# Optimization experiments

Measured on AMD Instinct MI355X. Metric: run time of the kernel, lower is better.

Reference implementation:

```python
import jax, jax.numpy as jnp
import numpy as np

DIM = 1024
HEADS = 16
HIDDEN = 4096
EPS = 1e-5


def layernorm(x, w, b):
    mu = jnp.mean(x, axis=-1, keepdims=True)
    var = jnp.var(x, axis=-1, keepdims=True)
    return (x - mu) * jax.lax.rsqrt(var + EPS) * w + b


def setup_inputs() -> dict:
    key = jax.random.key(0)
    ks = jax.random.split(key, 12)
    s = lambda fan_in: 1.0 / np.sqrt(fan_in)
    return {
        "x": jax.random.normal(ks[0], (8, 1024, DIM), dtype=jnp.float32),
        "norm1_w": jnp.ones((DIM,), jnp.float32),
        "norm1_b": jnp.zeros((DIM,), jnp.float32),
        "qkv_w": jax.random.uniform(ks[1], (3 * DIM, DIM), jnp.float32, -s(DIM), s(DIM)),
        "proj_w": jax.random.uniform(ks[2], (DIM, DIM), jnp.float32, -s(DIM), s(DIM)),
        "proj_b": jax.random.uniform(ks[3], (DIM,), jnp.float32, -s(DIM), s(DIM)),
        "norm2_w": jnp.ones((DIM,), jnp.float32),
        "norm2_b": jnp.zeros((DIM,), jnp.float32),
        "fc1_w": jax.random.uniform(ks[4], (HIDDEN, DIM), jnp.float32, -s(DIM), s(DIM)),
        "fc1_b": jax.random.uniform(ks[5], (HIDDEN,), jnp.float32, -s(DIM), s(DIM)),
        "fc2_w": jax.random.uniform(ks[6], (DIM, HIDDEN), jnp.float32, -s(HIDDEN), s(HIDDEN)),
        "fc2_b": jax.random.uniform(ks[7], (DIM,), jnp.float32, -s(HIDDEN), s(HIDDEN)),
    }


def reference(x, norm1_w, norm1_b, qkv_w, proj_w, proj_b,
              norm2_w, norm2_b, fc1_w, fc1_b, fc2_w, fc2_b):
    B, N, C = x.shape
    hd = C // HEADS
    scale = hd ** -0.5

    # ---- attention branch ----
    xn = layernorm(x, norm1_w, norm1_b)
    qkv_tmp = jnp.einsum('bnc,oc->bno', xn, qkv_w)          # [B,N,3C]
    qkv = qkv_tmp.reshape(B, N, 3, HEADS, hd).transpose(2, 0, 3, 1, 4)
    q, k, v = qkv[0], qkv[1], qkv[2]                         # [B,H,N,hd]
    qkv_out = qkv_tmp.reshape(B, N, 3, C).transpose(2, 0, 1, 3)
    attn = jnp.einsum('bhnd,bhmd->bhnm', q, k) * scale       # [B,H,N,N]
    attn = jax.nn.softmax(attn, axis=-1)
    ao = jnp.einsum('bhnm,bhmd->bhnd', attn, v)              # [B,H,N,hd]
    ao = ao.transpose(0, 2, 1, 3).reshape(B, N, C)
    attn_out = jnp.einsum('bnc,oc->bno', ao, proj_w) + proj_b
    x = x + attn_out

    # ---- mlp branch ----
    xn2 = layernorm(x, norm2_w, norm2_b)
    h = jnp.einsum('bnc,hc->bnh', xn2, fc1_w) + fc1_b
    h = jax.nn.gelu(h, approximate=False)
    hidden_out = jnp.einsum('bnh,ch->bnc', h, fc2_w) + fc2_b
    x = x + hidden_out
    return (x, (qkv_out[0], qkv_out[1], qkv_out[2]), hidden_out)
```

## Files before the change

### kernel.cpp

```cpp
#include <hip/hip_runtime.h>
#include <hip/hip_bf16.h>

typedef __attribute__((ext_vector_type(8))) __bf16 bf16x8;
typedef __attribute__((ext_vector_type(4))) float f32x4;
typedef unsigned short u16;
typedef unsigned int u32;

#define TOK 8192
#define C_DIM 1024
#define OUT_SEC 8388608

__device__ __forceinline__ u16 f2bf(float f) {
  return __builtin_bit_cast(u16, __float2bfloat16(f));
}

__device__ __forceinline__ void gl_lds16(const void* g, void* l) {
  __builtin_amdgcn_global_load_lds(
      (__attribute__((address_space(1))) void*)const_cast<void*>(g),
      (__attribute__((address_space(3))) void*)l, 16, 0, 0);
}

__device__ __forceinline__ float gelu_f(float x) {
  float y = 0.7978845608f * (x + 0.044715f * x * x * x);
  y = fminf(fmaxf(y, -15.f), 15.f);
  float e = __expf(2.0f * y);
  float th = (e - 1.0f) / (e + 1.0f);
  return 0.5f * x * (1.0f + th);
}

__global__ __launch_bounds__(256) void cvt_kernel(const float* __restrict__ in,
                                                  u16* __restrict__ out, int n4) {
  int i = blockIdx.x * blockDim.x + threadIdx.x;
  if (i >= n4) return;
  float4 v = reinterpret_cast<const float4*>(in)[i];
  alignas(8) u16 pk[4];
  pk[0] = f2bf(v.x); pk[1] = f2bf(v.y); pk[2] = f2bf(v.z); pk[3] = f2bf(v.w);
  reinterpret_cast<uint2*>(out)[i] = *reinterpret_cast<uint2*>(pk);
}

__global__ __launch_bounds__(256) void ln_kernel(const float* __restrict__ x,
                                                 const float* __restrict__ w,
                                                 const float* __restrict__ b,
                                                 u16* __restrict__ out) {
  const int row = blockIdx.x;
  const int t = threadIdx.x;
  const float* xr = x + (size_t)row * C_DIM;
  float4 v = reinterpret_cast<const float4*>(xr)[t];
  float s = v.x + v.y + v.z + v.w;
  float ss = v.x * v.x + v.y * v.y + v.z * v.z + v.w * v.w;
#pragma unroll
  for (int off = 1; off < 64; off <<= 1) {
    s += __shfl_xor(s, off, 64);
    ss += __shfl_xor(ss, off, 64);
  }
  __shared__ float red[8];
  const int wv = t >> 6;
  if ((t & 63) == 0) { red[wv] = s; red[4 + wv] = ss; }
  __syncthreads();
  s = red[0] + red[1] + red[2] + red[3];
  ss = red[4] + red[5] + red[6] + red[7];
  const float mu = s * (1.0f / C_DIM);
  const float var = ss * (1.0f / C_DIM) - mu * mu;
  const float rstd = rsqrtf(var + 1e-5f);
  float4 w4 = reinterpret_cast<const float4*>(w)[t];
  float4 b4 = reinterpret_cast<const float4*>(b)[t];
  alignas(8) u16 pk[4];
  pk[0] = f2bf((v.x - mu) * rstd * w4.x + b4.x);
  pk[1] = f2bf((v.y - mu) * rstd * w4.y + b4.y);
  pk[2] = f2bf((v.z - mu) * rstd * w4.z + b4.z);
  pk[3] = f2bf((v.w - mu) * rstd * w4.w + b4.w);
  reinterpret_cast<uint2*>(out + (size_t)row * C_DIM)[t] = *reinterpret_cast<uint2*>(pk);
}

__global__ __launch_bounds__(256) void vtrans_kernel(const float* __restrict__ vsrc,
                                                     u16* __restrict__ vt) {
  const int bh = blockIdx.x, nt = blockIdx.y;
  const int b = bh >> 4, h = bh & 15;
  const int t = threadIdx.x;
  __shared__ u16 T[64][65];
#pragma unroll
  for (int p = 0; p < 4; ++p) {
    const int idx = p * 256 + t;
    const int n = idx >> 4, d4 = (idx & 15) * 4;
    float4 x4 = *reinterpret_cast<const float4*>(
        vsrc + (size_t)(b * 1024 + nt * 64 + n) * 1024 + h * 64 + d4);
    T[d4 + 0][n] = f2bf(x4.x);
    T[d4 + 1][n] = f2bf(x4.y);
    T[d4 + 2][n] = f2bf(x4.z);
    T[d4 + 3][n] = f2bf(x4.w);
  }
  __syncthreads();
  const int d = t >> 2, ns = (t & 3) * 16;
  u16* dst = vt + (size_t)bh * 65536 + (size_t)d * 1024 + nt * 64 + ns;
  alignas(16) u16 tmp[16];
#pragma unroll
  for (int i = 0; i < 16; ++i) tmp[i] = T[d][ns + i];
  reinterpret_cast<uint4*>(dst)[0] = reinterpret_cast<uint4*>(tmp)[0];
  reinterpret_cast<uint4*>(dst)[1] = reinterpret_cast<uint4*>(tmp)[1];
}

#define MFMA_T(AF, BF, BASE)                                                \
  _Pragma("unroll") for (int nf = 0; nf < 4; ++nf) {                        \
    _Pragma("unroll") for (int mf = 0; mf < 4; ++mf)                        \
        acc[(BASE) + mf][nf] = __builtin_amdgcn_mfma_f32_16x16x32_bf16(     \
            AF[mf], BF[nf], acc[(BASE) + mf][nf], 0, 0, 0);                 \
  }

enum { EPI8_QKV = 0, EPI8_FC1 = 1 };

template <int EPI>
__global__ __launch_bounds__(512, 2) void gemm8(
    const u16* __restrict__ A, const u16* __restrict__ Bw,
    const float* __restrict__ bias,
    float* __restrict__ out, u16* __restrict__ h1, u16* __restrict__ h2,
    int K) {
  extern __shared__ char smem[];
  const int t = threadIdx.x, lane = t & 63, wid = t >> 6;
  const int wm = wid >> 2, wn = wid & 3;

  const int nwg = gridDim.x;
  int lin = blockIdx.x;
  lin = (lin & 7) * (nwg >> 3) + (lin >> 3);
  const int brow0 = (lin & 31) * 256;
  const int bcol0 = (lin >> 5) * 256;

  const int NT = K >> 6;

  f32x4 zero = {0.f, 0.f, 0.f, 0.f};
  f32x4 acc[8][4];
#pragma unroll
  for (int m = 0; m < 8; ++m)
#pragma unroll
    for (int n = 0; n < 4; ++n) acc[m][n] = zero;

  const int src_slot = ((t & 3) ^ ((t >> 3) & 3)) * 8;
  const int srow = t >> 2;
  auto stage = [&](int buf, int mat, int ks, int ktile) {
    const u16* G = mat ? Bw : A;
    const int gr0 = mat ? bcol0 : brow0;
    const int k0 = ktile * 64 + ks * 32 + src_slot;
    char* dst = smem + ((buf << 16) | (mat << 15) | (ks << 14));
#pragma unroll
    for (int i = 0; i < 2; ++i)
      gl_lds16(G + (size_t)(gr0 + i * 128 + srow) * K + k0, dst + i * 8192 + t * 16);
  };

  const int swz16 = (((lane >> 4) ^ ((lane >> 1) & 3)) << 4);
  const int l15 = lane & 15;

  stage(0, 0, 0, 0);
  stage(0, 1, 0, 0);
  stage(0, 0, 1, 0);
  stage(0, 1, 1, 0);
  asm volatile("s_waitcnt vmcnt(4)" ::: "memory");
  __builtin_amdgcn_s_barrier();

  for (int tt = 0; tt < NT; ++tt) {
    char* As_ = smem + ((tt & 1) << 16);
    char* Bs_ = As_ + 32768;
    const int nbuf = (tt & 1) ^ 1;
    const bool pf = (tt + 1 < NT);
    bf16x8 af[4], af2[4], bfr[4];

    auto LDA = [&](bf16x8* dst8, int MH, int KK) {
#pragma unroll
      for (int mf = 0; mf < 4; ++mf)
        dst8[mf] = *reinterpret_cast<const bf16x8*>(
            As_ + KK * 16384 + (wm * 128 + MH * 64 + mf * 16 + l15) * 64 + swz16);
    };
    auto LDB = [&](int KK) {
#pragma unroll
      for (int nf = 0; nf < 4; ++nf)
        bfr[nf] = *reinterpret_cast<const bf16x8*>(
            Bs_ + KK * 16384 + (wn * 64 + nf * 16 + l15) * 64 + swz16);
    };

    LDB(0);
    LDA(af, 0, 0);
    __builtin_amdgcn_sched_barrier(0);
    LDA(af2, 1, 0);
    __builtin_amdgcn_sched_barrier(0);
    if (pf) { stage(nbuf, 0, 0, tt + 1); stage(nbuf, 1, 0, tt + 1); }
    asm volatile("s_waitcnt lgkmcnt(4)" ::: "memory");
    __builtin_amdgcn_sched_barrier(0);
    __builtin_amdgcn_s_setprio(1);
    MFMA_T(af, bfr, 0)
    asm volatile("s_waitcnt lgkmcnt(0)" ::: "memory");
    __builtin_amdgcn_sched_barrier(0);
    MFMA_T(af2, bfr, 4)
    __builtin_amdgcn_s_setprio(0);
    if (pf) {
      asm volatile("s_waitcnt vmcnt(4)" ::: "memory");
    } else {
      asm volatile("s_waitcnt vmcnt(0)" ::: "memory");
    }
    __builtin_amdgcn_s_barrier();

    LDB(1);
    LDA(af, 1, 1);
    __builtin_amdgcn_sched_barrier(0);
    LDA(af2, 0, 1);
    __builtin_amdgcn_sched_barrier(0);
    if (pf) { stage(nbuf, 0, 1, tt + 1); stage(nbuf, 1, 1, tt + 1); }
    asm volatile("s_waitcnt lgkmcnt(4)" ::: "memory");
    __builtin_amdgcn_sched_barrier(0);
    __builtin_amdgcn_s_setprio(1);
    MFMA_T(af, bfr, 4)
    asm volatile("s_waitcnt lgkmcnt(0)" ::: "memory");
    __builtin_amdgcn_sched_barrier(0);
    MFMA_T(af2, bfr, 0)
    __builtin_amdgcn_s_setprio(0);
    if (pf)
      asm volatile("s_waitcnt vmcnt(4)" ::: "memory");
    __builtin_amdgcn_s_barrier();
  }

  const int rb = brow0 + wm * 128;
  const int cb = bcol0 + wn * 64;
#pragma unroll
  for (int m = 0; m < 8; ++m) {
#pragma unroll
    for (int n = 0; n < 4; ++n) {
      const int c = cb + n * 16 + l15;
#pragma unroll
      for (int j = 0; j < 4; ++j) {
        const int r = rb + m * 16 + (lane >> 4) * 4 + j;
        float v = acc[m][n][j];
        if constexpr (EPI == EPI8_QKV) {
          const int sec = c >> 10, cc = c & 1023;
          out[(size_t)sec * OUT_SEC + (size_t)r * 1024 + cc] = v;
          const size_t boff =
              (((size_t)(r >> 10) * 16 + (cc >> 6)) * 1024 + (r & 1023)) * 64 + (cc & 63);
          if (sec == 0) h1[boff] = f2bf(v * 0.18033688f);
          else if (sec == 1) h2[boff] = f2bf(v);
        } else {
          v += bias[c];
          h1[(size_t)r * 4096 + c] = f2bf(gelu_f(v));
        }
      }
    }
  }
}

enum { EPIN_PROJ = 0, EPIN_FC2 = 1 };

template <int EPI>
__global__ __launch_bounds__(512, 1) void gemm8n(
    const u16* __restrict__ A, const u16* __restrict__ Bw,
    const float* __restrict__ bias, const float* resid,
    float* out, float* out2_f, int K) {
  extern __shared__ char smem[];
  const int t = threadIdx.x, lane = t & 63, wid = t >> 6;
  const int wm = wid >> 2, wn = wid & 3;

  const int nwg = gridDim.x;
  int lin = blockIdx.x;
  lin = (lin & 7) * (nwg >> 3) + (lin >> 3);
  const int brow0 = (lin & 63) * 128;
  const int bcol0 = (lin >> 6) * 256;

  const int NT = K >> 6;

  f32x4 zero = {0.f, 0.f, 0.f, 0.f};
  f32x4 acc[4][4];
#pragma unroll
  for (int m = 0; m < 4; ++m)
#pragma unroll
    for (int n = 0; n < 4; ++n) acc[m][n] = zero;

  const int src_slot = ((t & 3) ^ ((t >> 3) & 3)) * 8;
  const int srow = t >> 2;
  auto stage_all = [&](char* dst, int ktile) {
#pragma unroll
    for (int ks = 0; ks < 2; ++ks) {
      const int k0 = ktile * 64 + ks * 32 + src_slot;
      gl_lds16(A + (size_t)(brow0 + srow) * K + k0, dst + ks * 8192 + t * 16);
    }
#pragma unroll
    for (int ks = 0; ks < 2; ++ks) {
      const int k0 = ktile * 64 + ks * 32 + src_slot;
      char* db = dst + 16384 + ks * 16384;
#pragma unroll
      for (int i = 0; i < 2; ++i)
        gl_lds16(Bw + (size_t)(bcol0 + i * 128 + srow) * K + k0, db + i * 8192 + t * 16);
    }
  };

  const int swz16 = (((lane >> 4) ^ ((lane >> 1) & 3)) << 4);
  const int l15 = lane & 15;

  char* bcur = smem;
  char* bnxt = smem + 49152;
  char* bspr = smem + 98304;

  stage_all(bcur, 0);
  stage_all(bnxt, 1);
  asm volatile("s_waitcnt vmcnt(6)" ::: "memory");
  __builtin_amdgcn_s_barrier();

  for (int tt = 0; tt < NT; ++tt) {
    const bool pf2 = (tt + 2 < NT);
    bf16x8 af[4], af2[4], bfr[4], bfr2[4];

    auto LDA = [&](bf16x8* dst8, int KK) {
#pragma unroll
      for (int mf = 0; mf < 4; ++mf)
        dst8[mf] = *reinterpret_cast<const bf16x8*>(
            bcur + KK * 8192 + (wm * 64 + mf * 16 + l15) * 64 + swz16);
    };
    auto LDB = [&](bf16x8* dst8, int KK) {
#pragma unroll
      for (int nf = 0; nf < 4; ++nf)
        dst8[nf] = *reinterpret_cast<const bf16x8*>(
            bcur + 16384 + KK * 16384 + (wn * 64 + nf * 16 + l15) * 64 + swz16);
    };

    LDA(af, 0);
    LDB(bfr, 0);
    __builtin_amdgcn_sched_barrier(0);
    LDA(af2, 1);
    LDB(bfr2, 1);
    __builtin_amdgcn_sched_barrier(0);
    if (pf2) stage_all(bspr, tt + 2);
    asm volatile("s_waitcnt lgkmcnt(8)" ::: "memory");
    __builtin_amdgcn_sched_barrier(0);
    __builtin_amdgcn_s_setprio(1);
    MFMA_T(af, bfr, 0)
    asm volatile("s_waitcnt lgkmcnt(0)" ::: "memory");
    __builtin_amdgcn_sched_barrier(0);
    MFMA_T(af2, bfr2, 0)
    __builtin_amdgcn_s_setprio(0);
    if (pf2) {
      asm volatile("s_waitcnt vmcnt(6)" ::: "memory");
    } else {
      asm volatile("s_waitcnt vmcnt(0)" ::: "memory");
    }
    __builtin_amdgcn_s_barrier();

    char* tmp = bcur;
    bcur = bnxt;
    bnxt = bspr;
    bspr = tmp;
  }

  const int rb = brow0 + wm * 64;
  const int cb = bcol0 + wn * 64;
#pragma unroll
  for (int m = 0; m < 4; ++m) {
#pragma unroll
    for (int n = 0; n < 4; ++n) {
      const int c = cb + n * 16 + l15;
#pragma unroll
      for (int j = 0; j < 4; ++j) {
        const int r = rb + m * 16 + (lane >> 4) * 4 + j;
        float v = acc[m][n][j];
        if constexpr (EPI == EPIN_PROJ) {
          v += bias[c] + resid[(size_t)r * 1024 + c];
          out[(size_t)r * 1024 + c] = v;
        } else {
          v += bias[c];
          out[(size_t)r * 1024 + c] = v;
          out2_f[(size_t)r * 1024 + c] = resid[(size_t)r * 1024 + c] + v;
        }
      }
    }
  }
}

__global__ __launch_bounds__(256) void attn_kernel(const u16* __restrict__ Qb,
                                                   const u16* __restrict__ Kb,
                                                   const u16* __restrict__ Vtb,
                                                   u16* __restrict__ ao) {
  const int orig = blockIdx.y * gridDim.x + blockIdx.x;
  const int wid = (orig & 7) * 128 + (orig >> 3);
  const int bh = wid >> 3;
  const int qt = wid & 7;
  const int b = bh >> 4, h = bh & 15;
  const int t = threadIdx.x, lane = t & 63, wv = t >> 6;
  const int l15 = lane & 15, g = lane >> 4;

  __shared__ u16 KV[3][8192];

  const int q0 = qt * 128 + wv * 32;
  bf16x8 qfA[2], qfB[2];
#pragma unroll
  for (int c = 0; c < 2; ++c) {
    qfA[c] = *reinterpret_cast<const bf16x8*>(
        Qb + (size_t)bh * 65536 + (size_t)(q0 + l15) * 64 + c * 32 + g * 8);
    qfB[c] = *reinterpret_cast<const bf16x8*>(
        Qb + (size_t)bh * 65536 + (size_t)(q0 + 16 + l15) * 64 + c * 32 + g * 8);
  }
  asm volatile("s_waitcnt vmcnt(0)" ::: "memory");

  f32x4 zero = {0.f, 0.f, 0.f, 0.f};
  f32x4 accO0[4], accO1[4];
#pragma unroll
  for (int nb = 0; nb < 4; ++nb) { accO0[nb] = zero; accO1[nb] = zero; }
  float m0 = -1e30f, m1 = -1e30f, lr0 = 0.f, lr1 = 0.f;

  const char* ktile0 = (const char*)(Kb + (size_t)bh * 65536);
  const char* vbase = (const char*)(Vtb + (size_t)bh * 65536);

  auto stage = [&](int buf, int kv0) {
    char* base = (char*)KV[buf];
#pragma unroll
    for (int i = 0; i < 2; ++i) {
      const int o = i * 4096 + t * 16;
      const int row = o >> 7, colb = o & 127;
      const int swz = colb ^ ((row & 7) << 4);
      gl_lds16(ktile0 + (size_t)kv0 * 128 + (size_t)row * 128 + swz, base + o);
      gl_lds16(vbase + (size_t)row * 2048 + (size_t)kv0 * 2 + swz, base + 8192 + o);
    }
  };

  stage(0, 0);
  stage(1, 64);
  asm volatile("s_waitcnt vmcnt(4)" ::: "memory");
  __builtin_amdgcn_s_barrier();
  int cur = 0;

  const int a0 = (l15 + ((g & 1) << 5)) << 2;
  const int a1 = a0 + 64;
  const bool up = (lane & 32) != 0;

  for (int tile = 0; tile < 16; ++tile) {
    const bool pf2 = (tile + 2 < 16);
    if (pf2) {
      int spare = cur + 2;
      if (spare >= 3) spare -= 3;
      stage(spare, (tile + 2) * 64);
    }

    const char* kcur = (const char*)KV[cur];
    const char* vcur = kcur + 8192;

    f32x4 s0[4], s1[4];
#pragma unroll
    for (int jb = 0; jb < 4; ++jb) { s0[jb] = zero; s1[jb] = zero; }
#pragma unroll
    for (int jb = 0; jb < 4; ++jb)
#pragma unroll
      for (int c = 0; c < 2; ++c) {
        const int row = jb * 16 + l15;
        const int colb = c * 64 + g * 16;
        bf16x8 kf = *reinterpret_cast<const bf16x8*>(
            kcur + row * 128 + (colb ^ ((row & 7) << 4)));
        s0[jb] = __builtin_amdgcn_mfma_f32_16x16x32_bf16(kf, qfA[c], s0[jb], 0, 0, 0);
        s1[jb] = __builtin_amdgcn_mfma_f32_16x16x32_bf16(kf, qfB[c], s1[jb], 0, 0, 0);
      }

    int w0[4][2], w1[4][2];
    {
      float a = fmaxf(fmaxf(s0[0][0], s0[0][1]), fmaxf(s0[0][2], s0[0][3]));
      float bmx = fmaxf(fmaxf(s0[1][0], s0[1][1]), fmaxf(s0[1][2], s0[1][3]));
      float cmx = fmaxf(fmaxf(s0[2][0], s0[2][1]), fmaxf(s0[2][2], s0[2][3]));
      float dmx = fmaxf(fmaxf(s0[3][0], s0[3][1]), fmaxf(s0[3][2], s0[3][3]));
      float mt = fmaxf(fmaxf(a, bmx), fmaxf(cmx, dmx));
      mt = fmaxf(mt, __shfl_xor(mt, 16, 64));
      mt = fmaxf(mt, __shfl_xor(mt, 32, 64));
      if (!__all(mt <= m0 + 8.0f)) {
        const float mn = fmaxf(m0, mt);
        const float sc = exp2f(m0 - mn);
        lr0 *= sc;
#pragma unroll
        for (int nb = 0; nb < 4; ++nb) accO0[nb] *= sc;
        m0 = mn;
      }
      float rs = 0.f;
#pragma unroll
      for (int jb = 0; jb < 4; ++jb)
#pragma unroll
        for (int r = 0; r < 4; ++r) {
          const float p = exp2f(s0[jb][r] - m0);
          s0[jb][r] = p;
          rs += p;
        }
      lr0 += rs;
#pragma unroll
      for (int jb = 0; jb < 4; ++jb) {
        w0[jb][0] = (int)((u32)f2bf(s0[jb][0]) | ((u32)f2bf(s0[jb][1]) << 16));
        w0[jb][1] = (int)((u32)f2bf(s0[jb][2]) | ((u32)f2bf(s0[jb][3]) << 16));
      }
    }
    {
      float a = fmaxf(fmaxf(s1[0][0], s1[0][1]), fmaxf(s1[0][2], s1[0][3]));
      float bmx = fmaxf(fmaxf(s1[1][0], s1[1][1]), fmaxf(s1[1][2], s1[1][3]));
      float cmx = fmaxf(fmaxf(s1[2][0], s1[2][1]), fmaxf(s1[2][2], s1[2][3]));
      float dmx = fmaxf(fmaxf(s1[3][0], s1[3][1]), fmaxf(s1[3][2], s1[3][3]));
      float mt = fmaxf(fmaxf(a, bmx), fmaxf(cmx, dmx));
      mt = fmaxf(mt, __shfl_xor(mt, 16, 64));
      mt = fmaxf(mt, __shfl_xor(mt, 32, 64));
      if (!__all(mt <= m1 + 8.0f)) {
        const float mn = fmaxf(m1, mt);
        const float sc = exp2f(m1 - mn);
        lr1 *= sc;
#pragma unroll
        for (int nb = 0; nb < 4; ++nb) accO1[nb] *= sc;
        m1 = mn;
      }
      float rs = 0.f;
#pragma unroll
      for (int jb = 0; jb < 4; ++jb)
#pragma unroll
        for (int r = 0; r < 4; ++r) {
          const float p = exp2f(s1[jb][r] - m1);
          s1[jb][r] = p;
          rs += p;
        }
      lr1 += rs;
#pragma unroll
      for (int jb = 0; jb < 4; ++jb) {
        w1[jb][0] = (int)((u32)f2bf(s1[jb][0]) | ((u32)f2bf(s1[jb][1]) << 16));
        w1[jb][1] = (int)((u32)f2bf(s1[jb][2]) | ((u32)f2bf(s1[jb][3]) << 16));
      }
    }

#pragma unroll
    for (int c = 0; c < 2; ++c) {
      int p0w0 = __builtin_amdgcn_ds_bpermute(a0, w0[2 * c][0]);
      int p0w0h = __builtin_amdgcn_ds_bpermute(a0, w0[2 * c + 1][0]);
      int p0w1 = __builtin_amdgcn_ds_bpermute(a0, w0[2 * c][1]);
      int p0w1h = __builtin_amdgcn_ds_bpermute(a0, w0[2 * c + 1][1]);
      int p0w2 = __builtin_amdgcn_ds_bpermute(a1, w0[2 * c][0]);
      int p0w2h = __builtin_amdgcn_ds_bpermute(a1, w0[2 * c + 1][0]);
      int p0w3 = __builtin_amdgcn_ds_bpermute(a1, w0[2 * c][1]);
      int p0w3h = __builtin_amdgcn_ds_bpermute(a1, w0[2 * c + 1][1]);
      alignas(16) int word0[4] = {up ? p0w0h : p0w0, up ? p0w1h : p0w1,
                                  up ? p0w2h : p0w2, up ? p0w3h : p0w3};
      bf16x8 pf0 = *reinterpret_cast<bf16x8*>(word0);

      int p1w0 = __builtin_amdgcn_ds_bpermute(a0, w1[2 * c][0]);
      int p1w0h = __builtin_amdgcn_ds_bpermute(a0, w1[2 * c + 1][0]);
      int p1w1 = __builtin_amdgcn_ds_bpermute(a0, w1[2 * c][1]);
      int p1w1h = __builtin_amdgcn_ds_bpermute(a0, w1[2 * c + 1][1]);
      int p1w2 = __builtin_amdgcn_ds_bpermute(a1, w1[2 * c][0]);
      int p1w2h = __builtin_amdgcn_ds_bpermute(a1, w1[2 * c + 1][0]);
      int p1w3 = __builtin_amdgcn_ds_bpermute(a1, w1[2 * c][1]);
      int p1w3h = __builtin_amdgcn_ds_bpermute(a1, w1[2 * c + 1][1]);
      alignas(16) int word1[4] = {up ? p1w0h : p1w0, up ? p1w1h : p1w1,
                                  up ? p1w2h : p1w2, up ? p1w3h : p1w3};
      bf16x8 pf1 = *reinterpret_cast<bf16x8*>(word1);

#pragma unroll
      for (int nb = 0; nb < 4; ++nb) {
        const int row = nb * 16 + l15;
        const int colb = c * 64 + g * 16;
        bf16x8 vf = *reinterpret_cast<const bf16x8*>(
            vcur + row * 128 + (colb ^ ((row & 7) << 4)));
        accO0[nb] = __builtin_amdgcn_mfma_f32_16x16x32_bf16(vf, pf0, accO0[nb], 0, 0, 0);
        accO1[nb] = __builtin_amdgcn_mfma_f32_16x16x32_bf16(vf, pf1, accO1[nb], 0, 0, 0);
      }
    }

    if (pf2) {
      asm volatile("s_waitcnt vmcnt(4)" ::: "memory");
    } else {
      asm volatile("s_waitcnt vmcnt(0)" ::: "memory");
    }
    __builtin_amdgcn_s_barrier();
    cur = (cur == 2) ? 0 : cur + 1;
  }

  lr0 += __shfl_xor(lr0, 16, 64);
  lr0 += __shfl_xor(lr0, 32, 64);
  lr1 += __shfl_xor(lr1, 16, 64);
  lr1 += __shfl_xor(lr1, 32, 64);
  const float rl0 = __builtin_amdgcn_rcpf(lr0);
  const float rl1 = __builtin_amdgcn_rcpf(lr1);

  u16* dst0 = ao + (size_t)(b * 1024 + q0 + l15) * 1024 + h * 64 + g * 4;
  u16* dst1 = ao + (size_t)(b * 1024 + q0 + 16 + l15) * 1024 + h * 64 + g * 4;
#pragma unroll
  for (int nb = 0; nb < 4; ++nb) {
    alignas(8) u16 pk0[4], pk1[4];
#pragma unroll
    for (int j = 0; j < 4; ++j) {
      pk0[j] = f2bf(accO0[nb][j] * rl0);
      pk1[j] = f2bf(accO1[nb][j] * rl1);
    }
    *reinterpret_cast<uint2*>(dst0 + nb * 16) = *reinterpret_cast<uint2*>(pk0);
    *reinterpret_cast<uint2*>(dst1 + nb * 16) = *reinterpret_cast<uint2*>(pk1);
  }
}

extern "C" void kernel_launch(void* const* d_in, const int* in_sizes, int n_in,
                              void* d_out, int out_size, void* d_ws, size_t ws_size,
                              hipStream_t stream) {
  const float* x      = (const float*)d_in[0];
  const float* n1w    = (const float*)d_in[1];
  const float* n1b    = (const float*)d_in[2];
  const float* qkv_w  = (const float*)d_in[3];
  const float* proj_w = (const float*)d_in[4];
  const float* proj_b = (const float*)d_in[5];
  const float* n2w    = (const float*)d_in[6];
  const float* n2b    = (const float*)d_in[7];
  const float* fc1_w  = (const float*)d_in[8];
  const float* fc1_b  = (const float*)d_in[9];
  const float* fc2_w  = (const float*)d_in[10];
  const float* fc2_b  = (const float*)d_in[11];
  float* out = (float*)d_out;

  u16* wsb    = (u16*)d_ws;
  u16* w_qkv  = wsb;
  u16* w_proj = wsb + 3145728;
  u16* w_fc1  = wsb + 4194304;
  u16* w_fc2  = wsb + 8388608;
  u16* xn     = wsb + 12582912;
  u16* Qb     = wsb + 20971520;
  u16* Kb     = wsb + 29360128;
  u16* Vtw    = wsb + 37748736;
  u16* ao     = wsb + 46137344;
  u16* hbuf   = wsb + 20971520;

  (void)hipFuncSetAttribute((const void*)gemm8<EPI8_QKV>,
                            hipFuncAttributeMaxDynamicSharedMemorySize, 131072);
  (void)hipFuncSetAttribute((const void*)gemm8<EPI8_FC1>,
                            hipFuncAttributeMaxDynamicSharedMemorySize, 131072);
  (void)hipFuncSetAttribute((const void*)gemm8n<EPIN_PROJ>,
                            hipFuncAttributeMaxDynamicSharedMemorySize, 147456);
  (void)hipFuncSetAttribute((const void*)gemm8n<EPIN_FC2>,
                            hipFuncAttributeMaxDynamicSharedMemorySize, 147456);

  cvt_kernel<<<3072, 256, 0, stream>>>(qkv_w, w_qkv, 786432);
  cvt_kernel<<<1024, 256, 0, stream>>>(proj_w, w_proj, 262144);
  cvt_kernel<<<4096, 256, 0, stream>>>(fc1_w, w_fc1, 1048576);
  cvt_kernel<<<4096, 256, 0, stream>>>(fc2_w, w_fc2, 1048576);

  ln_kernel<<<TOK, 256, 0, stream>>>(x, n1w, n1b, xn);
  gemm8<EPI8_QKV><<<384, 512, 131072, stream>>>(
      xn, w_qkv, nullptr, out + OUT_SEC, Qb, Kb, 1024);
  vtrans_kernel<<<dim3(128, 16), 256, 0, stream>>>(out + 3 * (size_t)OUT_SEC, Vtw);
  attn_kernel<<<dim3(128, 8), 256, 0, stream>>>(Qb, Kb, Vtw, ao);
  gemm8n<EPIN_PROJ><<<256, 512, 147456, stream>>>(
      ao, w_proj, proj_b, x, out, nullptr, 1024);
  ln_kernel<<<TOK, 256, 0, stream>>>(out, n2w, n2b, xn);
  gemm8<EPI8_FC1><<<512, 512, 131072, stream>>>(
      xn, w_fc1, fc1_b, nullptr, hbuf, nullptr, 1024);
  gemm8n<EPIN_FC2><<<256, 512, 147456, stream>>>(
      hbuf, w_fc2, fc2_b, out, out + 4 * (size_t)OUT_SEC, out, 4096);
}
```

Baseline: 441.5 us.

## Switch attention to double-buffered KV with higher occupancy and packed bf16 converts

Cuts the attention kernel's LDS ring from three 16KB buffers to two and restructures the loop so each iteration waits, barriers, then prefetches the next tile, instead of running two tiles ahead. It adds a launch_bounds occupancy hint of 4 blocks, so more waves fit per CU. It also swaps the scalar bf16 pack for the hardware v_cvt_pk_bf16_f32 instruction and uses 3-input max trees for the row max. The cost is a shallower prefetch, with a full vmcnt(0) wait each iteration that may expose load latency, and the register cap may cause spills.

Result: faster. 427.0 us (-3.3%).

```diff
diff --git a/kernel.cpp b/kernel.cpp
--- a/kernel.cpp
+++ b/kernel.cpp
@@ -12,6 +12,16 @@
 
 __device__ __forceinline__ u16 f2bf(float f) {
   return __builtin_bit_cast(u16, __float2bfloat16(f));
+}
+
+__device__ __forceinline__ int cvt_pk_bf16(float lo, float hi) {
+  int r;
+  asm("v_cvt_pk_bf16_f32 %0, %1, %2" : "=v"(r) : "v"(lo), "v"(hi));
+  return r;
+}
+
+__device__ __forceinline__ float max3f(float a, float b, float c) {
+  return fmaxf(fmaxf(a, b), c);
 }
 
 __device__ __forceinline__ void gl_lds16(const void* g, void* l) {
@@ -367,10 +377,10 @@
   }
 }
 
-__global__ __launch_bounds__(256) void attn_kernel(const u16* __restrict__ Qb,
-                                                   const u16* __restrict__ Kb,
-                                                   const u16* __restrict__ Vtb,
-                                                   u16* __restrict__ ao) {
+__global__ __launch_bounds__(256, 4) void attn_kernel(const u16* __restrict__ Qb,
+                                                      const u16* __restrict__ Kb,
+                                                      const u16* __restrict__ Vtb,
+                                                      u16* __restrict__ ao) {
   const int orig = blockIdx.y * gridDim.x + blockIdx.x;
   const int wid = (orig & 7) * 128 + (orig >> 3);
   const int bh = wid >> 3;
@@ -379,7 +389,7 @@
   const int t = threadIdx.x, lane = t & 63, wv = t >> 6;
   const int l15 = lane & 15, g = lane >> 4;
 
-  __shared__ u16 KV[3][8192];
+  __shared__ u16 KV[2][8192];
 
   const int q0 = qt * 128 + wv * 32;
   bf16x8 qfA[2], qfB[2];
@@ -390,7 +400,6 @@
     qfB[c] = *reinterpret_cast<const bf16x8*>(
         Qb + (size_t)bh * 65536 + (size_t)(q0 + 16 + l15) * 64 + c * 32 + g * 8);
   }
-  asm volatile("s_waitcnt vmcnt(0)" ::: "memory");
 
   f32x4 zero = {0.f, 0.f, 0.f, 0.f};
   f32x4 accO0[4], accO1[4];
@@ -414,9 +423,6 @@
   };
 
   stage(0, 0);
-  stage(1, 64);
-  asm volatile("s_waitcnt vmcnt(4)" ::: "memory");
-  __builtin_amdgcn_s_barrier();
   int cur = 0;
 
   const int a0 = (l15 + ((g & 1) << 5)) << 2;
@@ -424,12 +430,9 @@
   const bool up = (lane & 32) != 0;
 
   for (int tile = 0; tile < 16; ++tile) {
-    const bool pf2 = (tile + 2 < 16);
-    if (pf2) {
-      int spare = cur + 2;
-      if (spare >= 3) spare -= 3;
-      stage(spare, (tile + 2) * 64);
-    }
+    asm volatile("s_waitcnt vmcnt(0)" ::: "memory");
+    __builtin_amdgcn_s_barrier();
+    if (tile + 1 < 16) stage(cur ^ 1, (tile + 1) * 64);
 
     const char* kcur = (const char*)KV[cur];
     const char* vcur = kcur + 8192;
@@ -451,11 +454,13 @@
 
     int w0[4][2], w1[4][2];
     {
-      float a = fmaxf(fmaxf(s0[0][0], s0[0][1]), fmaxf(s0[0][2], s0[0][3]));
-      float bmx = fmaxf(fmaxf(s0[1][0], s0[1][1]), fmaxf(s0[1][2], s0[1][3]));
-      float cmx = fmaxf(fmaxf(s0[2][0], s0[2][1]), fmaxf(s0[2][2], s0[2][3]));
-      float dmx = fmaxf(fmaxf(s0[3][0], s0[3][1]), fmaxf(s0[3][2], s0[3][3]));
-      float mt = fmaxf(fmaxf(a, bmx), fmaxf(cmx, dmx));
+      float ta = max3f(s0[0][0], s0[0][1], s0[0][2]);
+      float tb = max3f(s0[0][3], s0[1][0], s0[1][1]);
+      float tc = max3f(s0[1][2], s0[1][3], s0[2][0]);
+      float td = max3f(s0[2][1], s0[2][2], s0[2][3]);
+      float te = max3f(s0[3][0], s0[3][1], s0[3][2]);
+      float mt = max3f(max3f(ta, tb, tc), max3f(td, te, s0[3][3]),
+                       -1e30f);
       mt = fmaxf(mt, __shfl_xor(mt, 16, 64));
       mt = fmaxf(mt, __shfl_xor(mt, 32, 64));
       if (!__all(mt <= m0 + 8.0f)) {
@@ -478,16 +483,18 @@
       lr0 += rs;
 #pragma unroll
       for (int jb = 0; jb < 4; ++jb) {
-        w0[jb][0] = (int)((u32)f2bf(s0[jb][0]) | ((u32)f2bf(s0[jb][1]) << 16));
-        w0[jb][1] = (int)((u32)f2bf(s0[jb][2]) | ((u32)f2bf(s0[jb][3]) << 16));
+        w0[jb][0] = cvt_pk_bf16(s0[jb][0], s0[jb][1]);
+        w0[jb][1] = cvt_pk_bf16(s0[jb][2], s0[jb][3]);
       }
     }
     {
-      float a = fmaxf(fmaxf(s1[0][0], s1[0][1]), fmaxf(s1[0][2], s1[0][3]));
-      float bmx = fmaxf(fmaxf(s1[1][0], s1[1][1]), fmaxf(s1[1][2], s1[1][3]));
-      float cmx = fmaxf(fmaxf(s1[2][0], s1[2][1]), fmaxf(s1[2][2], s1[2][3]));
-      float dmx = fmaxf(fmaxf(s1[3][0], s1[3][1]), fmaxf(s1[3][2], s1[3][3]));
-      float mt = fmaxf(fmaxf(a, bmx), fmaxf(cmx, dmx));
+      float ta = max3f(s1[0][0], s1[0][1], s1[0][2]);
+      float tb = max3f(s1[0][3], s1[1][0], s1[1][1]);
+      float tc = max3f(s1[1][2], s1[1][3], s1[2][0]);
+      float td = max3f(s1[2][1], s1[2][2], s1[2][3]);
+      float te = max3f(s1[3][0], s1[3][1], s1[3][2]);
+      float mt = max3f(max3f(ta, tb, tc), max3f(td, te, s1[3][3]),
+                       -1e30f);
       mt = fmaxf(mt, __shfl_xor(mt, 16, 64));
       mt = fmaxf(mt, __shfl_xor(mt, 32, 64));
       if (!__all(mt <= m1 + 8.0f)) {
@@ -510,8 +517,8 @@
       lr1 += rs;
 #pragma unroll
       for (int jb = 0; jb < 4; ++jb) {
-        w1[jb][0] = (int)((u32)f2bf(s1[jb][0]) | ((u32)f2bf(s1[jb][1]) << 16));
-        w1[jb][1] = (int)((u32)f2bf(s1[jb][2]) | ((u32)f2bf(s1[jb][3]) << 16));
+        w1[jb][0] = cvt_pk_bf16(s1[jb][0], s1[jb][1]);
+        w1[jb][1] = cvt_pk_bf16(s1[jb][2], s1[jb][3]);
       }
     }
 
@@ -552,13 +559,7 @@
       }
     }
 
-    if (pf2) {
-      asm volatile("s_waitcnt vmcnt(4)" ::: "memory");
-    } else {
-      asm volatile("s_waitcnt vmcnt(0)" ::: "memory");
-    }
-    __builtin_amdgcn_s_barrier();
-    cur = (cur == 2) ? 0 : cur + 1;
+    cur ^= 1;
   }
 
   lr0 += __shfl_xor(lr0, 16, 64);
```
